# Kernel tuning notes

Measured on AMD Instinct MI355X. Metric: run time of the kernel, lower is better.

The kernel has to match this reference:

```python
import jax, jax.numpy as jnp
import numpy as np
import math

NB_FEATURES = 256

def _softmax_kernel(x, projection_matrix):
    # x: [B,H,N,D], projection_matrix: [D,F] -> [B,H,N,F]
    x_proj = jnp.einsum('bhnd,df->bhnf', x, projection_matrix)
    x_proj = x_proj - jnp.max(x_proj, axis=-1, keepdims=True)
    return jnp.exp(x_proj) / math.sqrt(projection_matrix.shape[-1])

def setup_inputs() -> dict:
    key = jax.random.key(0)
    k1, k2, k3, k4 = jax.random.split(key, 4)
    B, H, N, D = 2, 16, 4096, 64
    q = jax.random.normal(k1, (B, H, N, D), dtype=jnp.float32)
    k = jax.random.normal(k2, (B, H, N, D), dtype=jnp.float32)
    v = jax.random.normal(k3, (B, H, N, D), dtype=jnp.float32)
    projection_matrix = jax.random.normal(k4, (D, NB_FEATURES), dtype=jnp.float32)
    return {"q": q, "k": k, "v": v, "projection_matrix": projection_matrix}

def reference(q, k, v, projection_matrix):
    q_prime = _softmax_kernel(q, projection_matrix)  # [B,H,N,F]
    k_prime = _softmax_kernel(k, projection_matrix)  # [B,H,N,F]
    kv = jnp.einsum('bhnf,bhne->bhfe', k_prime, v)   # [B,H,F,E]
    denom = jnp.einsum('bhnf,bhf->bhn', q_prime, jnp.sum(k_prime, axis=-2) + 1e-06)
    z = 1.0 / denom[..., None]                        # [B,H,N,1]
    out = jnp.einsum('bhnf,bhfe->bhne', q_prime, kv)  # [B,H,N,E]
    return out * z
```

## Files before the change

kernel.cpp:

```cpp
#include <hip/hip_runtime.h>
#include <math.h>

typedef float f4 __attribute__((ext_vector_type(4)));
typedef float f32x4 __attribute__((ext_vector_type(4)));
typedef _Float16 h4 __attribute__((ext_vector_type(4)));
typedef _Float16 h8 __attribute__((ext_vector_type(8)));

#define BH 32
#define NN 4096
#define DD 64
#define FF 256
#define EE 64
#define SPLITS 8
#define ROWS_K 512
#define QB 8
#define ROWS_Q 512
#define ST 72
#define SK 136
#define STF 264

#define MFMA(a, b, c) __builtin_amdgcn_mfma_f32_16x16x32_f16((a), (b), (c), 0, 0, 0)

__device__ inline h8 cvt2(f4 x0, f4 x1) {
  h8 r;
  r[0] = (_Float16)x0.x; r[1] = (_Float16)x0.y;
  r[2] = (_Float16)x0.z; r[3] = (_Float16)x0.w;
  r[4] = (_Float16)x1.x; r[5] = (_Float16)x1.y;
  r[6] = (_Float16)x1.z; r[7] = (_Float16)x1.w;
  return r;
}

__global__ __launch_bounds__(512, 2) void fa_kside(
    const float* __restrict__ kin, const float* __restrict__ vin,
    const float* __restrict__ P, float* __restrict__ kv_part,
    float* __restrict__ ksum_part) {
  __shared__ _Float16 Pt[FF * ST];
  __shared__ _Float16 kpt[FF * SK];
  __shared__ _Float16 vt[EE * SK];
  __shared__ float ks_lds[8 * FF];

  const int t = threadIdx.x;
  const int w = t >> 6, lane = t & 63;
  const int g = lane >> 4, fl = lane & 15;
  const int bh = blockIdx.x >> 3, split = blockIdx.x & 7;
  const int bhs = blockIdx.x;
  const int k0 = g * 8;

  {
    const f4* Pg4 = (const f4*)P;
#pragma unroll
    for (int i = 0; i < 8; ++i) {
      int idx = t + i * 512;
      f4 pv = Pg4[idx];
      int d = idx >> 6, f0 = (idx & 63) * 4;
      Pt[(f0 + 0) * ST + d] = (_Float16)pv.x;
      Pt[(f0 + 1) * ST + d] = (_Float16)pv.y;
      Pt[(f0 + 2) * ST + d] = (_Float16)pv.z;
      Pt[(f0 + 3) * ST + d] = (_Float16)pv.w;
    }
  }

  f32x4 kvacc[2][4];
#pragma unroll
  for (int mi = 0; mi < 2; ++mi)
#pragma unroll
    for (int nt = 0; nt < 4; ++nt) kvacc[mi][nt] = (f32x4){0.f, 0.f, 0.f, 0.f};
  float ksum_acc[16];
#pragma unroll
  for (int T = 0; T < 16; ++T) ksum_acc[T] = 0.f;

  const size_t base = (size_t)bh * NN * DD + (size_t)split * ROWS_K * DD;
  __syncthreads();

  for (int tile = 0; tile < 4; ++tile) {
    if (tile) __syncthreads();
    const int r0g = tile * 128 + w * 16;

    const float* krow = kin + base + (size_t)(r0g + fl) * DD;
    h8 a0 = cvt2(*(const f4*)&krow[k0], *(const f4*)&krow[k0 + 4]);
    h8 a1 = cvt2(*(const f4*)&krow[32 + k0], *(const f4*)&krow[32 + k0 + 4]);

    {
      const float* vb = vin + base + (size_t)r0g * DD + lane;
      h8 tv0, tv1;
#pragma unroll
      for (int j = 0; j < 8; ++j) tv0[j] = (_Float16)vb[j * DD];
#pragma unroll
      for (int j = 0; j < 8; ++j) tv1[j] = (_Float16)vb[(8 + j) * DD];
      *(h8*)&vt[lane * SK + w * 16] = tv0;
      *(h8*)&vt[lane * SK + w * 16 + 8] = tv1;
    }

    f32x4 lac[16];
#pragma unroll
    for (int T = 0; T < 16; ++T) {
      int ncol = T * 16 + fl;
      h8 b0 = *(const h8*)&Pt[ncol * ST + k0];
      h8 b1 = *(const h8*)&Pt[ncol * ST + 32 + k0];
      f32x4 c = {0.f, 0.f, 0.f, 0.f};
      c = MFMA(a0, b0, c);
      c = MFMA(a1, b1, c);
      lac[T] = c;
    }

    float mrow[4];
#pragma unroll
    for (int rg = 0; rg < 4; ++rg) {
      float m = lac[0][rg];
#pragma unroll
      for (int T = 1; T < 16; ++T) m = fmaxf(m, lac[T][rg]);
#pragma unroll
      for (int off = 1; off <= 8; off <<= 1)
        m = fmaxf(m, __shfl_xor(m, off, 64));
      mrow[rg] = m;
    }

#pragma unroll
    for (int T = 0; T < 16; ++T) {
      int ncol = T * 16 + fl;
      h4 kp;
#pragma unroll
      for (int rg = 0; rg < 4; ++rg) {
        float ev = __expf(lac[T][rg] - mrow[rg]) * 0.0625f;
        _Float16 hv = (_Float16)ev;
        ksum_acc[T] += (float)hv;
        kp[rg] = hv;
      }
      *(h4*)&kpt[ncol * SK + w * 16 + g * 4] = kp;
    }
    __syncthreads();

#pragma unroll
    for (int kst = 0; kst < 4; ++kst) {
      h8 vbf[4];
#pragma unroll
      for (int nt = 0; nt < 4; ++nt)
        vbf[nt] = *(const h8*)&vt[(nt * 16 + fl) * SK + kst * 32 + k0];
#pragma unroll
      for (int mi = 0; mi < 2; ++mi) {
        h8 ka = *(const h8*)&kpt[((2 * w + mi) * 16 + fl) * SK + kst * 32 + k0];
#pragma unroll
        for (int nt = 0; nt < 4; ++nt)
          kvacc[mi][nt] = MFMA(ka, vbf[nt], kvacc[mi][nt]);
      }
    }
  }

  float* kvp = kv_part + (size_t)bhs * (FF * EE);
#pragma unroll
  for (int mi = 0; mi < 2; ++mi)
#pragma unroll
    for (int nt = 0; nt < 4; ++nt)
#pragma unroll
      for (int rg = 0; rg < 4; ++rg) {
        int f = (2 * w + mi) * 16 + g * 4 + rg;
        int e = nt * 16 + fl;
        kvp[f * EE + e] = kvacc[mi][nt][rg];
      }

#pragma unroll
  for (int T = 0; T < 16; ++T) {
    float s = ksum_acc[T];
    s += __shfl_xor(s, 16, 64);
    s += __shfl_xor(s, 32, 64);
    if (lane < 16) ks_lds[w * FF + T * 16 + lane] = s;
  }
  __syncthreads();
  if (t < FF) {
    float s = 0.f;
#pragma unroll
    for (int wi = 0; wi < 8; ++wi) s += ks_lds[wi * FF + t];
    ksum_part[(size_t)bhs * FF + t] = s;
  }
}

__global__ __launch_bounds__(256) void fa_reduce(
    const float* __restrict__ kv_part, const float* __restrict__ ksum_part,
    _Float16* __restrict__ kvt_g, float* __restrict__ ksum_g) {
  __shared__ _Float16 tl[EE * 18];
  const int b = blockIdx.x, t = threadIdx.x;
  if (b < 512) {
    const int bh = b >> 4, c = b & 15;
#pragma unroll
    for (int i = 0; i < 4; ++i) {
      int idx = i * 256 + t;
      int fr = idx >> 6, e = idx & 63;
      float s = 0.f;
#pragma unroll
      for (int sp = 0; sp < SPLITS; ++sp)
        s += kv_part[(size_t)(bh * SPLITS + sp) * (FF * EE) + (c * 16 + fr) * EE + e];
      tl[e * 18 + fr] = (_Float16)s;
    }
    __syncthreads();
    unsigned int* og = (unsigned int*)kvt_g + (size_t)bh * 8192;
#pragma unroll
    for (int i = 0; i < 2; ++i) {
      int idx = i * 256 + t;
      int e = idx >> 3, fp = (idx & 7) * 2;
      og[e * 128 + c * 8 + (idx & 7)] = *(unsigned int*)&tl[e * 18 + fp];
    }
  } else {
    const int bh = b - 512;
    float s = 0.f;
#pragma unroll
    for (int sp = 0; sp < SPLITS; ++sp)
      s += ksum_part[(size_t)(bh * SPLITS + sp) * FF + t];
    ksum_g[bh * FF + t] = s + 1e-6f;
  }
}

__global__ __launch_bounds__(512, 2) void fa_qside(
    const float* __restrict__ qin, const float* __restrict__ P,
    const _Float16* __restrict__ kvt_g, const float* __restrict__ ksum_g,
    float* __restrict__ out) {
  __shared__ _Float16 Pt[FF * ST];
  __shared__ _Float16 kvt[EE * STF];
  __shared__ _Float16 qpt[8 * 16 * STF];

  const int t = threadIdx.x;
  const int w = t >> 6, lane = t & 63;
  const int g = lane >> 4, fl = lane & 15;
  const int bh = blockIdx.x >> 3, qb = blockIdx.x & 7;
  const int k0 = g * 8;

  {
    const f4* Pg4 = (const f4*)P;
#pragma unroll
    for (int i = 0; i < 8; ++i) {
      int idx = t + i * 512;
      f4 pv = Pg4[idx];
      int d = idx >> 6, f0 = (idx & 63) * 4;
      Pt[(f0 + 0) * ST + d] = (_Float16)pv.x;
      Pt[(f0 + 1) * ST + d] = (_Float16)pv.y;
      Pt[(f0 + 2) * ST + d] = (_Float16)pv.z;
      Pt[(f0 + 3) * ST + d] = (_Float16)pv.w;
    }
  }
  {
    const h8* src = (const h8*)(kvt_g + (size_t)bh * FF * EE);
#pragma unroll
    for (int i = 0; i < 4; ++i) {
      int idx = t + i * 512;
      int e = idx >> 5, f0 = (idx & 31) * 8;
      *(h8*)&kvt[e * STF + f0] = src[idx];
    }
  }
  float ksr[16];
#pragma unroll
  for (int T = 0; T < 16; ++T) ksr[T] = ksum_g[bh * FF + T * 16 + fl];
  __syncthreads();

  _Float16* myqpt = qpt + w * 16 * STF;
  const size_t base = (size_t)bh * NN * DD + (size_t)qb * ROWS_Q * DD;
  float* ob = out + (size_t)bh * NN * EE + (size_t)qb * ROWS_Q * EE;

  for (int st = 0; st < 4; ++st) {
    const int r0g = st * 128 + w * 16;
    const float* qrow = qin + base + (size_t)(r0g + fl) * DD;
    h8 a0 = cvt2(*(const f4*)&qrow[k0], *(const f4*)&qrow[k0 + 4]);
    h8 a1 = cvt2(*(const f4*)&qrow[32 + k0], *(const f4*)&qrow[32 + k0 + 4]);

    f32x4 lac[16];
#pragma unroll
    for (int T = 0; T < 16; ++T) {
      int ncol = T * 16 + fl;
      h8 b0 = *(const h8*)&Pt[ncol * ST + k0];
      h8 b1 = *(const h8*)&Pt[ncol * ST + 32 + k0];
      f32x4 c = {0.f, 0.f, 0.f, 0.f};
      c = MFMA(a0, b0, c);
      c = MFMA(a1, b1, c);
      lac[T] = c;
    }

    float mrow[4];
#pragma unroll
    for (int rg = 0; rg < 4; ++rg) {
      float m = lac[0][rg];
#pragma unroll
      for (int T = 1; T < 16; ++T) m = fmaxf(m, lac[T][rg]);
#pragma unroll
      for (int off = 1; off <= 8; off <<= 1)
        m = fmaxf(m, __shfl_xor(m, off, 64));
      mrow[rg] = m;
    }

    float den[4] = {0.f, 0.f, 0.f, 0.f};
#pragma unroll
    for (int T = 0; T < 16; ++T) {
      int ncol = T * 16 + fl;
#pragma unroll
      for (int rg = 0; rg < 4; ++rg) {
        float ev = __expf(lac[T][rg] - mrow[rg]) * 0.0625f;
        _Float16 hv = (_Float16)ev;
        den[rg] += (float)hv * ksr[T];
        myqpt[(g * 4 + rg) * STF + ncol] = hv;
      }
    }
#pragma unroll
    for (int rg = 0; rg < 4; ++rg) {
#pragma unroll
      for (int off = 1; off <= 8; off <<= 1)
        den[rg] += __shfl_xor(den[rg], off, 64);
    }

    f32x4 oacc[4];
#pragma unroll
    for (int nt = 0; nt < 4; ++nt) oacc[nt] = (f32x4){0.f, 0.f, 0.f, 0.f};
#pragma unroll
    for (int kst = 0; kst < 8; ++kst) {
      h8 aq = *(const h8*)&myqpt[fl * STF + kst * 32 + k0];
#pragma unroll
      for (int nt = 0; nt < 4; ++nt) {
        h8 bq = *(const h8*)&kvt[(nt * 16 + fl) * STF + kst * 32 + k0];
        oacc[nt] = MFMA(aq, bq, oacc[nt]);
      }
    }

    float* obt = ob + (size_t)r0g * EE;
#pragma unroll
    for (int rg = 0; rg < 4; ++rg) {
      float inv = 1.0f / den[rg];
#pragma unroll
      for (int nt = 0; nt < 4; ++nt) {
        int e = nt * 16 + fl;
        obt[(g * 4 + rg) * EE + e] = oacc[nt][rg] * inv;
      }
    }
  }
}

extern "C" void kernel_launch(void* const* d_in, const int* in_sizes, int n_in,
                              void* d_out, int out_size, void* d_ws,
                              size_t ws_size, hipStream_t stream) {
  (void)in_sizes;
  (void)n_in;
  (void)out_size;
  (void)ws_size;
  const float* q = (const float*)d_in[0];
  const float* k = (const float*)d_in[1];
  const float* v = (const float*)d_in[2];
  const float* P = (const float*)d_in[3];
  float* out = (float*)d_out;

  float* kv_part = (float*)d_ws;
  float* ksum_part = kv_part + 256 * 16384;
  _Float16* kvt_g = (_Float16*)(ksum_part + 256 * 256);
  float* ksum_g = (float*)(kvt_g + 32 * 16384);

  hipLaunchKernelGGL(fa_kside, dim3(BH * SPLITS), dim3(512), 0, stream, k, v, P,
                     kv_part, ksum_part);
  hipLaunchKernelGGL(fa_reduce, dim3(544), dim3(256), 0, stream, kv_part,
                     ksum_part, kvt_g, ksum_g);
  hipLaunchKernelGGL(fa_qside, dim3(BH * QB), dim3(512), 0, stream, q, P, kvt_g,
                     ksum_g, out);
}
```

Before: 174.8 us.

## Double block size by splitting feature dimension across wave pairs

Both the k-side and q-side kernels now launch 1024 threads (16 waves) instead of 512. Each pair of waves shares a 16-row strip and each wave handles half of the 256 features. The row max and the denominator are combined across the pair through small LDS buffers plus extra barriers. The goal is more resident waves per CU, since LDS already limits each CU to one block, so that latency is hidden better. The cost is extra __syncthreads and LDS traffic per tile, and the launch-bounds hint may squeeze registers.

```diff
diff --git a/kernel.cpp b/kernel.cpp
--- a/kernel.cpp
+++ b/kernel.cpp
@@ -30,27 +30,30 @@
   return r;
 }
 
-__global__ __launch_bounds__(512, 2) void fa_kside(
+__global__ __launch_bounds__(1024, 4) void fa_kside(
     const float* __restrict__ kin, const float* __restrict__ vin,
     const float* __restrict__ P, float* __restrict__ kv_part,
     float* __restrict__ ksum_part) {
   __shared__ _Float16 Pt[FF * ST];
   __shared__ _Float16 kpt[FF * SK];
   __shared__ _Float16 vt[EE * SK];
-  __shared__ float ks_lds[8 * FF];
+  __shared__ float mx_lds[8 * 32];
+  __shared__ float ks_lds[16 * 128];
 
   const int t = threadIdx.x;
   const int w = t >> 6, lane = t & 63;
   const int g = lane >> 4, fl = lane & 15;
+  const int s = w >> 1, h = w & 1;
   const int bh = blockIdx.x >> 3, split = blockIdx.x & 7;
   const int bhs = blockIdx.x;
   const int k0 = g * 8;
+  const int fbase = h * 128;
 
   {
     const f4* Pg4 = (const f4*)P;
 #pragma unroll
-    for (int i = 0; i < 8; ++i) {
-      int idx = t + i * 512;
+    for (int i = 0; i < 4; ++i) {
+      int idx = t + i * 1024;
       f4 pv = Pg4[idx];
       int d = idx >> 6, f0 = (idx & 63) * 4;
       Pt[(f0 + 0) * ST + d] = (_Float16)pv.x;
@@ -60,41 +63,36 @@
     }
   }
 
-  f32x4 kvacc[2][4];
-#pragma unroll
-  for (int mi = 0; mi < 2; ++mi)
-#pragma unroll
-    for (int nt = 0; nt < 4; ++nt) kvacc[mi][nt] = (f32x4){0.f, 0.f, 0.f, 0.f};
-  float ksum_acc[16];
-#pragma unroll
-  for (int T = 0; T < 16; ++T) ksum_acc[T] = 0.f;
+  f32x4 kvacc[4];
+#pragma unroll
+  for (int nt = 0; nt < 4; ++nt) kvacc[nt] = (f32x4){0.f, 0.f, 0.f, 0.f};
+  float ksum_acc[8];
+#pragma unroll
+  for (int T = 0; T < 8; ++T) ksum_acc[T] = 0.f;
 
   const size_t base = (size_t)bh * NN * DD + (size_t)split * ROWS_K * DD;
   __syncthreads();
 
   for (int tile = 0; tile < 4; ++tile) {
     if (tile) __syncthreads();
-    const int r0g = tile * 128 + w * 16;
-
-    const float* krow = kin + base + (size_t)(r0g + fl) * DD;
+    const int r0 = tile * 128;
+
+    const float* krow = kin + base + (size_t)(r0 + s * 16 + fl) * DD;
     h8 a0 = cvt2(*(const f4*)&krow[k0], *(const f4*)&krow[k0 + 4]);
     h8 a1 = cvt2(*(const f4*)&krow[32 + k0], *(const f4*)&krow[32 + k0 + 4]);
 
     {
-      const float* vb = vin + base + (size_t)r0g * DD + lane;
-      h8 tv0, tv1;
-#pragma unroll
-      for (int j = 0; j < 8; ++j) tv0[j] = (_Float16)vb[j * DD];
-#pragma unroll
-      for (int j = 0; j < 8; ++j) tv1[j] = (_Float16)vb[(8 + j) * DD];
-      *(h8*)&vt[lane * SK + w * 16] = tv0;
-      *(h8*)&vt[lane * SK + w * 16 + 8] = tv1;
-    }
-
-    f32x4 lac[16];
-#pragma unroll
-    for (int T = 0; T < 16; ++T) {
-      int ncol = T * 16 + fl;
+      const float* vb = vin + base + (size_t)(r0 + w * 8) * DD + lane;
+      h8 tv;
+#pragma unroll
+      for (int j = 0; j < 8; ++j) tv[j] = (_Float16)vb[j * DD];
+      *(h8*)&vt[lane * SK + w * 8] = tv;
+    }
+
+    f32x4 lac[8];
+#pragma unroll
+    for (int T = 0; T < 8; ++T) {
+      int ncol = fbase + T * 16 + fl;
       h8 b0 = *(const h8*)&Pt[ncol * ST + k0];
       h8 b1 = *(const h8*)&Pt[ncol * ST + 32 + k0];
       f32x4 c = {0.f, 0.f, 0.f, 0.f};
@@ -108,16 +106,25 @@
     for (int rg = 0; rg < 4; ++rg) {
       float m = lac[0][rg];
 #pragma unroll
-      for (int T = 1; T < 16; ++T) m = fmaxf(m, lac[T][rg]);
+      for (int T = 1; T < 8; ++T) m = fmaxf(m, lac[T][rg]);
 #pragma unroll
       for (int off = 1; off <= 8; off <<= 1)
         m = fmaxf(m, __shfl_xor(m, off, 64));
       mrow[rg] = m;
     }
-
-#pragma unroll
-    for (int T = 0; T < 16; ++T) {
-      int ncol = T * 16 + fl;
+    if (fl == 0) {
+#pragma unroll
+      for (int rg = 0; rg < 4; ++rg)
+        mx_lds[s * 32 + h * 16 + g * 4 + rg] = mrow[rg];
+    }
+    __syncthreads();
+#pragma unroll
+    for (int rg = 0; rg < 4; ++rg)
+      mrow[rg] = fmaxf(mrow[rg], mx_lds[s * 32 + (1 - h) * 16 + g * 4 + rg]);
+
+#pragma unroll
+    for (int T = 0; T < 8; ++T) {
+      int ncol = fbase + T * 16 + fl;
       h4 kp;
 #pragma unroll
       for (int rg = 0; rg < 4; ++rg) {
@@ -126,7 +133,7 @@
         ksum_acc[T] += (float)hv;
         kp[rg] = hv;
       }
-      *(h4*)&kpt[ncol * SK + w * 16 + g * 4] = kp;
+      *(h4*)&kpt[ncol * SK + s * 16 + g * 4] = kp;
     }
     __syncthreads();
 
@@ -136,41 +143,37 @@
 #pragma unroll
       for (int nt = 0; nt < 4; ++nt)
         vbf[nt] = *(const h8*)&vt[(nt * 16 + fl) * SK + kst * 32 + k0];
-#pragma unroll
-      for (int mi = 0; mi < 2; ++mi) {
-        h8 ka = *(const h8*)&kpt[((2 * w + mi) * 16 + fl) * SK + kst * 32 + k0];
-#pragma unroll
-        for (int nt = 0; nt < 4; ++nt)
-          kvacc[mi][nt] = MFMA(ka, vbf[nt], kvacc[mi][nt]);
-      }
+      h8 ka = *(const h8*)&kpt[(w * 16 + fl) * SK + kst * 32 + k0];
+#pragma unroll
+      for (int nt = 0; nt < 4; ++nt)
+        kvacc[nt] = MFMA(ka, vbf[nt], kvacc[nt]);
     }
   }
 
   float* kvp = kv_part + (size_t)bhs * (FF * EE);
 #pragma unroll
-  for (int mi = 0; mi < 2; ++mi)
-#pragma unroll
-    for (int nt = 0; nt < 4; ++nt)
-#pragma unroll
-      for (int rg = 0; rg < 4; ++rg) {
-        int f = (2 * w + mi) * 16 + g * 4 + rg;
-        int e = nt * 16 + fl;
-        kvp[f * EE + e] = kvacc[mi][nt][rg];
-      }
-
-#pragma unroll
-  for (int T = 0; T < 16; ++T) {
-    float s = ksum_acc[T];
-    s += __shfl_xor(s, 16, 64);
-    s += __shfl_xor(s, 32, 64);
-    if (lane < 16) ks_lds[w * FF + T * 16 + lane] = s;
+  for (int nt = 0; nt < 4; ++nt)
+#pragma unroll
+    for (int rg = 0; rg < 4; ++rg) {
+      int f = w * 16 + g * 4 + rg;
+      int e = nt * 16 + fl;
+      kvp[f * EE + e] = kvacc[nt][rg];
+    }
+
+#pragma unroll
+  for (int T = 0; T < 8; ++T) {
+    float sv = ksum_acc[T];
+    sv += __shfl_xor(sv, 16, 64);
+    sv += __shfl_xor(sv, 32, 64);
+    if (lane < 16) ks_lds[w * 128 + T * 16 + lane] = sv;
   }
   __syncthreads();
   if (t < FF) {
-    float s = 0.f;
-#pragma unroll
-    for (int wi = 0; wi < 8; ++wi) s += ks_lds[wi * FF + t];
-    ksum_part[(size_t)bhs * FF + t] = s;
+    int hh = t >> 7, inner = t & 127;
+    float sv = 0.f;
+#pragma unroll
+    for (int si = 0; si < 8; ++si) sv += ks_lds[(si * 2 + hh) * 128 + inner];
+    ksum_part[(size_t)bhs * FF + t] = sv;
   }
 }
 
@@ -209,25 +212,29 @@
   }
 }
 
-__global__ __launch_bounds__(512, 2) void fa_qside(
+__global__ __launch_bounds__(1024, 4) void fa_qside(
     const float* __restrict__ qin, const float* __restrict__ P,
     const _Float16* __restrict__ kvt_g, const float* __restrict__ ksum_g,
     float* __restrict__ out) {
   __shared__ _Float16 Pt[FF * ST];
   __shared__ _Float16 kvt[EE * STF];
   __shared__ _Float16 qpt[8 * 16 * STF];
+  __shared__ float mx_lds[8 * 32];
+  __shared__ float den_lds[8 * 32];
 
   const int t = threadIdx.x;
   const int w = t >> 6, lane = t & 63;
   const int g = lane >> 4, fl = lane & 15;
+  const int s = w >> 1, h = w & 1;
   const int bh = blockIdx.x >> 3, qb = blockIdx.x & 7;
   const int k0 = g * 8;
+  const int fbase = h * 128;
 
   {
     const f4* Pg4 = (const f4*)P;
 #pragma unroll
-    for (int i = 0; i < 8; ++i) {
-      int idx = t + i * 512;
+    for (int i = 0; i < 4; ++i) {
+      int idx = t + i * 1024;
       f4 pv = Pg4[idx];
       int d = idx >> 6, f0 = (idx & 63) * 4;
       Pt[(f0 + 0) * ST + d] = (_Float16)pv.x;
@@ -239,31 +246,33 @@
   {
     const h8* src = (const h8*)(kvt_g + (size_t)bh * FF * EE);
 #pragma unroll
-    for (int i = 0; i < 4; ++i) {
-      int idx = t + i * 512;
+    for (int i = 0; i < 2; ++i) {
+      int idx = t + i * 1024;
       int e = idx >> 5, f0 = (idx & 31) * 8;
       *(h8*)&kvt[e * STF + f0] = src[idx];
     }
   }
-  float ksr[16];
-#pragma unroll
-  for (int T = 0; T < 16; ++T) ksr[T] = ksum_g[bh * FF + T * 16 + fl];
+  float ksr[8];
+#pragma unroll
+  for (int T = 0; T < 8; ++T)
+    ksr[T] = ksum_g[bh * FF + fbase + T * 16 + fl];
   __syncthreads();
 
-  _Float16* myqpt = qpt + w * 16 * STF;
+  _Float16* myqpt = qpt + s * 16 * STF;
   const size_t base = (size_t)bh * NN * DD + (size_t)qb * ROWS_Q * DD;
   float* ob = out + (size_t)bh * NN * EE + (size_t)qb * ROWS_Q * EE;
 
   for (int st = 0; st < 4; ++st) {
-    const int r0g = st * 128 + w * 16;
-    const float* qrow = qin + base + (size_t)(r0g + fl) * DD;
+    if (st) __syncthreads();
+    const int r0 = st * 128;
+    const float* qrow = qin + base + (size_t)(r0 + s * 16 + fl) * DD;
     h8 a0 = cvt2(*(const f4*)&qrow[k0], *(const f4*)&qrow[k0 + 4]);
     h8 a1 = cvt2(*(const f4*)&qrow[32 + k0], *(const f4*)&qrow[32 + k0 + 4]);
 
-    f32x4 lac[16];
-#pragma unroll
-    for (int T = 0; T < 16; ++T) {
-      int ncol = T * 16 + fl;
+    f32x4 lac[8];
+#pragma unroll
+    for (int T = 0; T < 8; ++T) {
+      int ncol = fbase + T * 16 + fl;
       h8 b0 = *(const h8*)&Pt[ncol * ST + k0];
       h8 b1 = *(const h8*)&Pt[ncol * ST + 32 + k0];
       f32x4 c = {0.f, 0.f, 0.f, 0.f};
@@ -277,17 +286,26 @@
     for (int rg = 0; rg < 4; ++rg) {
       float m = lac[0][rg];
 #pragma unroll
-      for (int T = 1; T < 16; ++T) m = fmaxf(m, lac[T][rg]);
+      for (int T = 1; T < 8; ++T) m = fmaxf(m, lac[T][rg]);
 #pragma unroll
       for (int off = 1; off <= 8; off <<= 1)
         m = fmaxf(m, __shfl_xor(m, off, 64));
       mrow[rg] = m;
     }
+    if (fl == 0) {
+#pragma unroll
+      for (int rg = 0; rg < 4; ++rg)
+        mx_lds[s * 32 + h * 16 + g * 4 + rg] = mrow[rg];
+    }
+    __syncthreads();
+#pragma unroll
+    for (int rg = 0; rg < 4; ++rg)
+      mrow[rg] = fmaxf(mrow[rg], mx_lds[s * 32 + (1 - h) * 16 + g * 4 + rg]);
 
     float den[4] = {0.f, 0.f, 0.f, 0.f};
 #pragma unroll
-    for (int T = 0; T < 16; ++T) {
-      int ncol = T * 16 + fl;
+    for (int T = 0; T < 8; ++T) {
+      int ncol = fbase + T * 16 + fl;
 #pragma unroll
       for (int rg = 0; rg < 4; ++rg) {
         float ev = __expf(lac[T][rg] - mrow[rg]) * 0.0625f;
@@ -302,28 +320,40 @@
       for (int off = 1; off <= 8; off <<= 1)
         den[rg] += __shfl_xor(den[rg], off, 64);
     }
-
-    f32x4 oacc[4];
-#pragma unroll
-    for (int nt = 0; nt < 4; ++nt) oacc[nt] = (f32x4){0.f, 0.f, 0.f, 0.f};
+    if (fl == 0) {
+#pragma unroll
+      for (int rg = 0; rg < 4; ++rg)
+        den_lds[s * 32 + h * 16 + g * 4 + rg] = den[rg];
+    }
+    __syncthreads();
+
+    float inv[4];
+#pragma unroll
+    for (int rg = 0; rg < 4; ++rg) {
+      float dtot = den_lds[s * 32 + g * 4 + rg] + den_lds[s * 32 + 16 + g * 4 + rg];
+      inv[rg] = 1.0f / dtot;
+    }
+
+    f32x4 oacc[2];
+#pragma unroll
+    for (int n2 = 0; n2 < 2; ++n2) oacc[n2] = (f32x4){0.f, 0.f, 0.f, 0.f};
 #pragma unroll
     for (int kst = 0; kst < 8; ++kst) {
       h8 aq = *(const h8*)&myqpt[fl * STF + kst * 32 + k0];
 #pragma unroll
-      for (int nt = 0; nt < 4; ++nt) {
-        h8 bq = *(const h8*)&kvt[(nt * 16 + fl) * STF + kst * 32 + k0];
-        oacc[nt] = MFMA(aq, bq, oacc[nt]);
+      for (int n2 = 0; n2 < 2; ++n2) {
+        h8 bq = *(const h8*)&kvt[((h * 2 + n2) * 16 + fl) * STF + kst * 32 + k0];
+        oacc[n2] = MFMA(aq, bq, oacc[n2]);
       }
     }
 
-    float* obt = ob + (size_t)r0g * EE;
-#pragma unroll
-    for (int rg = 0; rg < 4; ++rg) {
-      float inv = 1.0f / den[rg];
-#pragma unroll
-      for (int nt = 0; nt < 4; ++nt) {
-        int e = nt * 16 + fl;
-        obt[(g * 4 + rg) * EE + e] = oacc[nt][rg] * inv;
+    float* obt = ob + (size_t)(r0 + s * 16) * EE;
+#pragma unroll
+    for (int rg = 0; rg < 4; ++rg) {
+#pragma unroll
+      for (int n2 = 0; n2 < 2; ++n2) {
+        int e = (h * 2 + n2) * 16 + fl;
+        obt[(g * 4 + rg) * EE + e] = oacc[n2][rg] * inv[rg];
       }
     }
   }
@@ -347,10 +377,10 @@
   _Float16* kvt_g = (_Float16*)(ksum_part + 256 * 256);
   float* ksum_g = (float*)(kvt_g + 32 * 16384);
 
-  hipLaunchKernelGGL(fa_kside, dim3(BH * SPLITS), dim3(512), 0, stream, k, v, P,
-                     kv_part, ksum_part);
+  hipLaunchKernelGGL(fa_kside, dim3(BH * SPLITS), dim3(1024), 0, stream, k, v,
+                     P, kv_part, ksum_part);
   hipLaunchKernelGGL(fa_reduce, dim3(544), dim3(256), 0, stream, kv_part,
                      ksum_part, kvt_g, ksum_g);
-  hipLaunchKernelGGL(fa_qside, dim3(BH * QB), dim3(512), 0, stream, q, P, kvt_g,
-                     ksum_g, out);
-}
+  hipLaunchKernelGGL(fa_qside, dim3(BH * QB), dim3(1024), 0, stream, q, P,
+                     kvt_g, ksum_g, out);
+}
```

Measured after the change: 182.1 us. +4.2%, slower.

## Double splits, store fp16 KV partials, keep Q features in registers

Applied to the files above, without the earlier changes.

The K-side kernel now runs 512 blocks of 256 threads over 256-row splits, with an XOR-swizzled LDS layout for the exp(K) tile and KV partials written in fp16. This halves the partial traffic into the reduce step. The Q-side kernel swaps the MFMA operands so each lane holds a full output row's features in registers. The second GEMM uses 16x16x16 MFMA directly from registers, which removes the per-wave LDS staging of q features and lets the kernel target higher occupancy. fp16 partial sums add some rounding error, and the larger split count doubles the reduce's read count.

```diff
diff --git a/kernel.cpp b/kernel.cpp
--- a/kernel.cpp
+++ b/kernel.cpp
@@ -11,15 +11,15 @@
 #define DD 64
 #define FF 256
 #define EE 64
-#define SPLITS 8
-#define ROWS_K 512
-#define QB 8
-#define ROWS_Q 512
+#define SPLITS 16
+#define ROWS_K 256
+#define QB 16
+#define ROWS_Q 256
 #define ST 72
-#define SK 136
 #define STF 264
 
 #define MFMA(a, b, c) __builtin_amdgcn_mfma_f32_16x16x32_f16((a), (b), (c), 0, 0, 0)
+#define MFMA16(a, b, c) __builtin_amdgcn_mfma_f32_16x16x16f16((a), (b), (c), 0, 0, 0)
 
 __device__ inline h8 cvt2(f4 x0, f4 x1) {
   h8 r;
@@ -30,20 +30,204 @@
   return r;
 }
 
-__global__ __launch_bounds__(512, 2) void fa_kside(
+__global__ __launch_bounds__(256, 2) void fa_kside(
     const float* __restrict__ kin, const float* __restrict__ vin,
-    const float* __restrict__ P, float* __restrict__ kv_part,
+    const float* __restrict__ P, _Float16* __restrict__ kv_part,
     float* __restrict__ ksum_part) {
   __shared__ _Float16 Pt[FF * ST];
-  __shared__ _Float16 kpt[FF * SK];
-  __shared__ _Float16 vt[EE * SK];
-  __shared__ float ks_lds[8 * FF];
+  __shared__ _Float16 kpt[FF * 64];
+  __shared__ _Float16 vt[EE * 72];
+  float* ks_lds = (float*)vt;
 
   const int t = threadIdx.x;
   const int w = t >> 6, lane = t & 63;
   const int g = lane >> 4, fl = lane & 15;
-  const int bh = blockIdx.x >> 3, split = blockIdx.x & 7;
+  const int bh = blockIdx.x >> 4, split = blockIdx.x & 15;
   const int bhs = blockIdx.x;
+  const int k0 = g * 8;
+  const int swz = (fl & 7) << 3;
+
+  {
+    const f4* Pg4 = (const f4*)P;
+#pragma unroll
+    for (int i = 0; i < 16; ++i) {
+      int idx = t + i * 256;
+      f4 pv = Pg4[idx];
+      int d = idx >> 6, f0 = (idx & 63) * 4;
+      Pt[(f0 + 0) * ST + d] = (_Float16)pv.x;
+      Pt[(f0 + 1) * ST + d] = (_Float16)pv.y;
+      Pt[(f0 + 2) * ST + d] = (_Float16)pv.z;
+      Pt[(f0 + 3) * ST + d] = (_Float16)pv.w;
+    }
+  }
+
+  f32x4 kvacc[4][4];
+#pragma unroll
+  for (int mi = 0; mi < 4; ++mi)
+#pragma unroll
+    for (int nt = 0; nt < 4; ++nt) kvacc[mi][nt] = (f32x4){0.f, 0.f, 0.f, 0.f};
+  float ksum_acc[16];
+#pragma unroll
+  for (int T = 0; T < 16; ++T) ksum_acc[T] = 0.f;
+
+  const size_t base = (size_t)bh * NN * DD + (size_t)split * ROWS_K * DD;
+  __syncthreads();
+
+  for (int tile = 0; tile < 4; ++tile) {
+    if (tile) __syncthreads();
+    const int r0g = tile * 64 + w * 16;
+
+    const float* krow = kin + base + (size_t)(r0g + fl) * DD;
+    h8 a0 = cvt2(*(const f4*)&krow[k0], *(const f4*)&krow[k0 + 4]);
+    h8 a1 = cvt2(*(const f4*)&krow[32 + k0], *(const f4*)&krow[32 + k0 + 4]);
+
+    {
+      const float* vb = vin + base + (size_t)r0g * DD + lane;
+      h8 tv0, tv1;
+#pragma unroll
+      for (int j = 0; j < 8; ++j) tv0[j] = (_Float16)vb[j * DD];
+#pragma unroll
+      for (int j = 0; j < 8; ++j) tv1[j] = (_Float16)vb[(8 + j) * DD];
+      *(h8*)&vt[lane * 72 + w * 16] = tv0;
+      *(h8*)&vt[lane * 72 + w * 16 + 8] = tv1;
+    }
+
+    f32x4 lac[16];
+#pragma unroll
+    for (int T = 0; T < 16; ++T) {
+      int ncol = T * 16 + fl;
+      h8 b0 = *(const h8*)&Pt[ncol * ST + k0];
+      h8 b1 = *(const h8*)&Pt[ncol * ST + 32 + k0];
+      f32x4 c = {0.f, 0.f, 0.f, 0.f};
+      c = MFMA(a0, b0, c);
+      c = MFMA(a1, b1, c);
+      lac[T] = c;
+    }
+
+    float mrow[4];
+#pragma unroll
+    for (int rg = 0; rg < 4; ++rg) {
+      float m = lac[0][rg];
+#pragma unroll
+      for (int T = 1; T < 16; ++T) m = fmaxf(m, lac[T][rg]);
+#pragma unroll
+      for (int off = 1; off <= 8; off <<= 1)
+        m = fmaxf(m, __shfl_xor(m, off, 64));
+      mrow[rg] = m;
+    }
+
+    const int kcol = (w * 16 + g * 4) ^ swz;
+#pragma unroll
+    for (int T = 0; T < 16; ++T) {
+      int ncol = T * 16 + fl;
+      h4 kp;
+#pragma unroll
+      for (int rg = 0; rg < 4; ++rg) {
+        float ev = __expf(lac[T][rg] - mrow[rg]) * 0.0625f;
+        _Float16 hv = (_Float16)ev;
+        ksum_acc[T] += (float)hv;
+        kp[rg] = hv;
+      }
+      *(h4*)&kpt[ncol * 64 + kcol] = kp;
+    }
+    __syncthreads();
+
+    const int rc0 = (0 * 32 + k0) ^ swz;
+    const int rc1 = (1 * 32 + k0) ^ swz;
+#pragma unroll
+    for (int kst = 0; kst < 2; ++kst) {
+      const int rcs = kst ? rc1 : rc0;
+      h8 vbf[4];
+#pragma unroll
+      for (int nt = 0; nt < 4; ++nt)
+        vbf[nt] = *(const h8*)&vt[(nt * 16 + fl) * 72 + kst * 32 + k0];
+#pragma unroll
+      for (int mi = 0; mi < 4; ++mi) {
+        h8 ka = *(const h8*)&kpt[((4 * w + mi) * 16 + fl) * 64 + rcs];
+#pragma unroll
+        for (int nt = 0; nt < 4; ++nt)
+          kvacc[mi][nt] = MFMA(ka, vbf[nt], kvacc[mi][nt]);
+      }
+    }
+  }
+
+  _Float16* kvp = kv_part + (size_t)bhs * (FF * EE);
+#pragma unroll
+  for (int mi = 0; mi < 4; ++mi)
+#pragma unroll
+    for (int nt = 0; nt < 4; ++nt)
+#pragma unroll
+      for (int rg = 0; rg < 4; ++rg) {
+        int f = (4 * w + mi) * 16 + g * 4 + rg;
+        int e = nt * 16 + fl;
+        kvp[f * EE + e] = (_Float16)kvacc[mi][nt][rg];
+      }
+
+  __syncthreads();
+#pragma unroll
+  for (int T = 0; T < 16; ++T) {
+    float s = ksum_acc[T];
+    s += __shfl_xor(s, 16, 64);
+    s += __shfl_xor(s, 32, 64);
+    if (lane < 16) ks_lds[w * FF + T * 16 + lane] = s;
+  }
+  __syncthreads();
+  {
+    float s = 0.f;
+#pragma unroll
+    for (int wi = 0; wi < 4; ++wi) s += ks_lds[wi * FF + t];
+    ksum_part[(size_t)bhs * FF + t] = s;
+  }
+}
+
+__global__ __launch_bounds__(256) void fa_reduce(
+    const _Float16* __restrict__ kv_part, const float* __restrict__ ksum_part,
+    _Float16* __restrict__ kvt_g, float* __restrict__ ksum_g) {
+  __shared__ _Float16 tl[EE * 18];
+  const int b = blockIdx.x, t = threadIdx.x;
+  if (b < 512) {
+    const int bh = b >> 4, c = b & 15;
+#pragma unroll
+    for (int i = 0; i < 4; ++i) {
+      int idx = i * 256 + t;
+      int fr = idx >> 6, e = idx & 63;
+      float s = 0.f;
+#pragma unroll
+      for (int sp = 0; sp < SPLITS; ++sp)
+        s += (float)kv_part[(size_t)(bh * SPLITS + sp) * (FF * EE) +
+                            (c * 16 + fr) * EE + e];
+      tl[e * 18 + fr] = (_Float16)s;
+    }
+    __syncthreads();
+    unsigned int* og = (unsigned int*)kvt_g + (size_t)bh * 8192;
+#pragma unroll
+    for (int i = 0; i < 2; ++i) {
+      int idx = i * 256 + t;
+      int e = idx >> 3, fp = (idx & 7) * 2;
+      og[e * 128 + c * 8 + (idx & 7)] = *(unsigned int*)&tl[e * 18 + fp];
+    }
+  } else {
+    const int bh = b - 512;
+    float s = 0.f;
+#pragma unroll
+    for (int sp = 0; sp < SPLITS; ++sp)
+      s += ksum_part[(size_t)(bh * SPLITS + sp) * FF + t];
+    ksum_g[bh * FF + t] = s + 1e-6f;
+  }
+}
+
+__global__ __launch_bounds__(512, 4) void fa_qside(
+    const float* __restrict__ qin, const float* __restrict__ P,
+    const _Float16* __restrict__ kvt_g, const float* __restrict__ ksum_g,
+    float* __restrict__ out) {
+  __shared__ _Float16 Pt[FF * ST];
+  __shared__ _Float16 kvt[EE * STF];
+  __shared__ float ks_lds[FF];
+
+  const int t = threadIdx.x;
+  const int w = t >> 6, lane = t & 63;
+  const int g = lane >> 4, fl = lane & 15;
+  const int bh = blockIdx.x >> 4, qb = blockIdx.x & 15;
   const int k0 = g * 8;
 
   {
@@ -59,37 +243,26 @@
       Pt[(f0 + 3) * ST + d] = (_Float16)pv.w;
     }
   }
-
-  f32x4 kvacc[2][4];
-#pragma unroll
-  for (int mi = 0; mi < 2; ++mi)
-#pragma unroll
-    for (int nt = 0; nt < 4; ++nt) kvacc[mi][nt] = (f32x4){0.f, 0.f, 0.f, 0.f};
-  float ksum_acc[16];
-#pragma unroll
-  for (int T = 0; T < 16; ++T) ksum_acc[T] = 0.f;
-
-  const size_t base = (size_t)bh * NN * DD + (size_t)split * ROWS_K * DD;
+  {
+    const h8* src = (const h8*)(kvt_g + (size_t)bh * FF * EE);
+#pragma unroll
+    for (int i = 0; i < 4; ++i) {
+      int idx = t + i * 512;
+      int e = idx >> 5, f0 = (idx & 31) * 8;
+      *(h8*)&kvt[e * STF + f0] = src[idx];
+    }
+  }
+  if (t < FF) ks_lds[t] = ksum_g[bh * FF + t];
   __syncthreads();
 
-  for (int tile = 0; tile < 4; ++tile) {
-    if (tile) __syncthreads();
-    const int r0g = tile * 128 + w * 16;
-
-    const float* krow = kin + base + (size_t)(r0g + fl) * DD;
-    h8 a0 = cvt2(*(const f4*)&krow[k0], *(const f4*)&krow[k0 + 4]);
-    h8 a1 = cvt2(*(const f4*)&krow[32 + k0], *(const f4*)&krow[32 + k0 + 4]);
-
-    {
-      const float* vb = vin + base + (size_t)r0g * DD + lane;
-      h8 tv0, tv1;
-#pragma unroll
-      for (int j = 0; j < 8; ++j) tv0[j] = (_Float16)vb[j * DD];
-#pragma unroll
-      for (int j = 0; j < 8; ++j) tv1[j] = (_Float16)vb[(8 + j) * DD];
-      *(h8*)&vt[lane * SK + w * 16] = tv0;
-      *(h8*)&vt[lane * SK + w * 16 + 8] = tv1;
-    }
+  const size_t base = (size_t)bh * NN * DD + (size_t)qb * ROWS_Q * DD;
+  float* ob = out + (size_t)bh * NN * EE + (size_t)qb * ROWS_Q * EE;
+
+  for (int st = 0; st < 2; ++st) {
+    const int r0g = st * 128 + w * 16;
+    const float* qrow = qin + base + (size_t)(r0g + fl) * DD;
+    h8 a0 = cvt2(*(const f4*)&qrow[k0], *(const f4*)&qrow[k0 + 4]);
+    h8 a1 = cvt2(*(const f4*)&qrow[32 + k0], *(const f4*)&qrow[32 + k0 + 4]);
 
     f32x4 lac[16];
 #pragma unroll
@@ -98,233 +271,55 @@
       h8 b0 = *(const h8*)&Pt[ncol * ST + k0];
       h8 b1 = *(const h8*)&Pt[ncol * ST + 32 + k0];
       f32x4 c = {0.f, 0.f, 0.f, 0.f};
-      c = MFMA(a0, b0, c);
-      c = MFMA(a1, b1, c);
+      c = MFMA(b0, a0, c);
+      c = MFMA(b1, a1, c);
       lac[T] = c;
     }
 
-    float mrow[4];
-#pragma unroll
-    for (int rg = 0; rg < 4; ++rg) {
-      float m = lac[0][rg];
-#pragma unroll
-      for (int T = 1; T < 16; ++T) m = fmaxf(m, lac[T][rg]);
-#pragma unroll
-      for (int off = 1; off <= 8; off <<= 1)
-        m = fmaxf(m, __shfl_xor(m, off, 64));
-      mrow[rg] = m;
-    }
-
+    float m = lac[0][0];
+#pragma unroll
+    for (int T = 0; T < 16; ++T)
+#pragma unroll
+      for (int rg = 0; rg < 4; ++rg) m = fmaxf(m, lac[T][rg]);
+    m = fmaxf(m, __shfl_xor(m, 16, 64));
+    m = fmaxf(m, __shfl_xor(m, 32, 64));
+
+    h4 qp4[16];
+    float den = 0.f;
 #pragma unroll
     for (int T = 0; T < 16; ++T) {
-      int ncol = T * 16 + fl;
-      h4 kp;
+      f4 ksf = *(const f4*)&ks_lds[T * 16 + g * 4];
 #pragma unroll
       for (int rg = 0; rg < 4; ++rg) {
-        float ev = __expf(lac[T][rg] - mrow[rg]) * 0.0625f;
+        float ev = __expf(lac[T][rg] - m) * 0.0625f;
         _Float16 hv = (_Float16)ev;
-        ksum_acc[T] += (float)hv;
-        kp[rg] = hv;
-      }
-      *(h4*)&kpt[ncol * SK + w * 16 + g * 4] = kp;
-    }
-    __syncthreads();
-
-#pragma unroll
-    for (int kst = 0; kst < 4; ++kst) {
-      h8 vbf[4];
-#pragma unroll
-      for (int nt = 0; nt < 4; ++nt)
-        vbf[nt] = *(const h8*)&vt[(nt * 16 + fl) * SK + kst * 32 + k0];
-#pragma unroll
-      for (int mi = 0; mi < 2; ++mi) {
-        h8 ka = *(const h8*)&kpt[((2 * w + mi) * 16 + fl) * SK + kst * 32 + k0];
-#pragma unroll
-        for (int nt = 0; nt < 4; ++nt)
-          kvacc[mi][nt] = MFMA(ka, vbf[nt], kvacc[mi][nt]);
-      }
-    }
-  }
-
-  float* kvp = kv_part + (size_t)bhs * (FF * EE);
-#pragma unroll
-  for (int mi = 0; mi < 2; ++mi)
-#pragma unroll
-    for (int nt = 0; nt < 4; ++nt)
-#pragma unroll
-      for (int rg = 0; rg < 4; ++rg) {
-        int f = (2 * w + mi) * 16 + g * 4 + rg;
-        int e = nt * 16 + fl;
-        kvp[f * EE + e] = kvacc[mi][nt][rg];
-      }
-
-#pragma unroll
-  for (int T = 0; T < 16; ++T) {
-    float s = ksum_acc[T];
-    s += __shfl_xor(s, 16, 64);
-    s += __shfl_xor(s, 32, 64);
-    if (lane < 16) ks_lds[w * FF + T * 16 + lane] = s;
-  }
-  __syncthreads();
-  if (t < FF) {
-    float s = 0.f;
-#pragma unroll
-    for (int wi = 0; wi < 8; ++wi) s += ks_lds[wi * FF + t];
-    ksum_part[(size_t)bhs * FF + t] = s;
-  }
-}
-
-__global__ __launch_bounds__(256) void fa_reduce(
-    const float* __restrict__ kv_part, const float* __restrict__ ksum_part,
-    _Float16* __restrict__ kvt_g, float* __restrict__ ksum_g) {
-  __shared__ _Float16 tl[EE * 18];
-  const int b = blockIdx.x, t = threadIdx.x;
-  if (b < 512) {
-    const int bh = b >> 4, c = b & 15;
-#pragma unroll
-    for (int i = 0; i < 4; ++i) {
-      int idx = i * 256 + t;
-      int fr = idx >> 6, e = idx & 63;
-      float s = 0.f;
-#pragma unroll
-      for (int sp = 0; sp < SPLITS; ++sp)
-        s += kv_part[(size_t)(bh * SPLITS + sp) * (FF * EE) + (c * 16 + fr) * EE + e];
-      tl[e * 18 + fr] = (_Float16)s;
-    }
-    __syncthreads();
-    unsigned int* og = (unsigned int*)kvt_g + (size_t)bh * 8192;
-#pragma unroll
-    for (int i = 0; i < 2; ++i) {
-      int idx = i * 256 + t;
-      int e = idx >> 3, fp = (idx & 7) * 2;
-      og[e * 128 + c * 8 + (idx & 7)] = *(unsigned int*)&tl[e * 18 + fp];
-    }
-  } else {
-    const int bh = b - 512;
-    float s = 0.f;
-#pragma unroll
-    for (int sp = 0; sp < SPLITS; ++sp)
-      s += ksum_part[(size_t)(bh * SPLITS + sp) * FF + t];
-    ksum_g[bh * FF + t] = s + 1e-6f;
-  }
-}
-
-__global__ __launch_bounds__(512, 2) void fa_qside(
-    const float* __restrict__ qin, const float* __restrict__ P,
-    const _Float16* __restrict__ kvt_g, const float* __restrict__ ksum_g,
-    float* __restrict__ out) {
-  __shared__ _Float16 Pt[FF * ST];
-  __shared__ _Float16 kvt[EE * STF];
-  __shared__ _Float16 qpt[8 * 16 * STF];
-
-  const int t = threadIdx.x;
-  const int w = t >> 6, lane = t & 63;
-  const int g = lane >> 4, fl = lane & 15;
-  const int bh = blockIdx.x >> 3, qb = blockIdx.x & 7;
-  const int k0 = g * 8;
-
-  {
-    const f4* Pg4 = (const f4*)P;
-#pragma unroll
-    for (int i = 0; i < 8; ++i) {
-      int idx = t + i * 512;
-      f4 pv = Pg4[idx];
-      int d = idx >> 6, f0 = (idx & 63) * 4;
-      Pt[(f0 + 0) * ST + d] = (_Float16)pv.x;
-      Pt[(f0 + 1) * ST + d] = (_Float16)pv.y;
-      Pt[(f0 + 2) * ST + d] = (_Float16)pv.z;
-      Pt[(f0 + 3) * ST + d] = (_Float16)pv.w;
-    }
-  }
-  {
-    const h8* src = (const h8*)(kvt_g + (size_t)bh * FF * EE);
-#pragma unroll
-    for (int i = 0; i < 4; ++i) {
-      int idx = t + i * 512;
-      int e = idx >> 5, f0 = (idx & 31) * 8;
-      *(h8*)&kvt[e * STF + f0] = src[idx];
-    }
-  }
-  float ksr[16];
-#pragma unroll
-  for (int T = 0; T < 16; ++T) ksr[T] = ksum_g[bh * FF + T * 16 + fl];
-  __syncthreads();
-
-  _Float16* myqpt = qpt + w * 16 * STF;
-  const size_t base = (size_t)bh * NN * DD + (size_t)qb * ROWS_Q * DD;
-  float* ob = out + (size_t)bh * NN * EE + (size_t)qb * ROWS_Q * EE;
-
-  for (int st = 0; st < 4; ++st) {
-    const int r0g = st * 128 + w * 16;
-    const float* qrow = qin + base + (size_t)(r0g + fl) * DD;
-    h8 a0 = cvt2(*(const f4*)&qrow[k0], *(const f4*)&qrow[k0 + 4]);
-    h8 a1 = cvt2(*(const f4*)&qrow[32 + k0], *(const f4*)&qrow[32 + k0 + 4]);
-
-    f32x4 lac[16];
-#pragma unroll
-    for (int T = 0; T < 16; ++T) {
-      int ncol = T * 16 + fl;
-      h8 b0 = *(const h8*)&Pt[ncol * ST + k0];
-      h8 b1 = *(const h8*)&Pt[ncol * ST + 32 + k0];
-      f32x4 c = {0.f, 0.f, 0.f, 0.f};
-      c = MFMA(a0, b0, c);
-      c = MFMA(a1, b1, c);
-      lac[T] = c;
-    }
-
-    float mrow[4];
-#pragma unroll
-    for (int rg = 0; rg < 4; ++rg) {
-      float m = lac[0][rg];
-#pragma unroll
-      for (int T = 1; T < 16; ++T) m = fmaxf(m, lac[T][rg]);
-#pragma unroll
-      for (int off = 1; off <= 8; off <<= 1)
-        m = fmaxf(m, __shfl_xor(m, off, 64));
-      mrow[rg] = m;
-    }
-
-    float den[4] = {0.f, 0.f, 0.f, 0.f};
-#pragma unroll
-    for (int T = 0; T < 16; ++T) {
-      int ncol = T * 16 + fl;
-#pragma unroll
-      for (int rg = 0; rg < 4; ++rg) {
-        float ev = __expf(lac[T][rg] - mrow[rg]) * 0.0625f;
-        _Float16 hv = (_Float16)ev;
-        den[rg] += (float)hv * ksr[T];
-        myqpt[(g * 4 + rg) * STF + ncol] = hv;
-      }
-    }
-#pragma unroll
-    for (int rg = 0; rg < 4; ++rg) {
-#pragma unroll
-      for (int off = 1; off <= 8; off <<= 1)
-        den[rg] += __shfl_xor(den[rg], off, 64);
-    }
+        den += (float)hv * ksf[rg];
+        qp4[T][rg] = hv;
+      }
+    }
+    den += __shfl_xor(den, 16, 64);
+    den += __shfl_xor(den, 32, 64);
+    const float inv = 1.0f / den;
 
     f32x4 oacc[4];
 #pragma unroll
     for (int nt = 0; nt < 4; ++nt) oacc[nt] = (f32x4){0.f, 0.f, 0.f, 0.f};
 #pragma unroll
-    for (int kst = 0; kst < 8; ++kst) {
-      h8 aq = *(const h8*)&myqpt[fl * STF + kst * 32 + k0];
+    for (int kst = 0; kst < 16; ++kst) {
 #pragma unroll
       for (int nt = 0; nt < 4; ++nt) {
-        h8 bq = *(const h8*)&kvt[(nt * 16 + fl) * STF + kst * 32 + k0];
-        oacc[nt] = MFMA(aq, bq, oacc[nt]);
-      }
-    }
-
-    float* obt = ob + (size_t)r0g * EE;
-#pragma unroll
-    for (int rg = 0; rg < 4; ++rg) {
-      float inv = 1.0f / den[rg];
-#pragma unroll
-      for (int nt = 0; nt < 4; ++nt) {
-        int e = nt * 16 + fl;
-        obt[(g * 4 + rg) * EE + e] = oacc[nt][rg] * inv;
-      }
+        h4 av = *(const h4*)&kvt[(nt * 16 + fl) * STF + kst * 16 + g * 4];
+        oacc[nt] = MFMA16(av, qp4[kst], oacc[nt]);
+      }
+    }
+
+    float* obt = ob + (size_t)(r0g + fl) * EE;
+#pragma unroll
+    for (int nt = 0; nt < 4; ++nt) {
+      f4 o;
+#pragma unroll
+      for (int rg = 0; rg < 4; ++rg) o[rg] = oacc[nt][rg] * inv;
+      *(f4*)&obt[nt * 16 + g * 4] = o;
     }
   }
 }
@@ -342,12 +337,12 @@
   const float* P = (const float*)d_in[3];
   float* out = (float*)d_out;
 
-  float* kv_part = (float*)d_ws;
-  float* ksum_part = kv_part + 256 * 16384;
-  _Float16* kvt_g = (_Float16*)(ksum_part + 256 * 256);
+  _Float16* kv_part = (_Float16*)d_ws;
+  float* ksum_part = (float*)(kv_part + 512 * 16384);
+  _Float16* kvt_g = (_Float16*)(ksum_part + 512 * 256);
   float* ksum_g = (float*)(kvt_g + 32 * 16384);
 
-  hipLaunchKernelGGL(fa_kside, dim3(BH * SPLITS), dim3(512), 0, stream, k, v, P,
+  hipLaunchKernelGGL(fa_kside, dim3(BH * SPLITS), dim3(256), 0, stream, k, v, P,
                      kv_part, ksum_part);
   hipLaunchKernelGGL(fa_reduce, dim3(544), dim3(256), 0, stream, kv_part,
                      ksum_part, kvt_g, ksum_g);
```

New measurement: 344.1 us. 1.97x slower.

## Split K-side into 16 chunks of 256-thread blocks with fp16 partials and swizzled LDS

Applied to the files above, without the earlier changes.

Restructures the K-side kernel to use 16 splits of 256 rows with 256-thread blocks, each wave now accumulating 64 feature rows of the kv partial. The kv partials are stored as fp16 instead of fp32 to halve the partial write and reduce traffic, and the k' LDS tile drops its padding in favour of an XOR swizzle to avoid bank conflicts. The ksum scratch reuses the V tile buffer to cut LDS use. It doubles the number of partials the reduce kernel sums and adds fp16 rounding to the partial sums.

```diff
diff --git a/kernel.cpp b/kernel.cpp
--- a/kernel.cpp
+++ b/kernel.cpp
@@ -11,12 +11,11 @@
 #define DD 64
 #define FF 256
 #define EE 64
-#define SPLITS 8
-#define ROWS_K 512
+#define SPLITS 16
+#define ROWS_K 256
 #define QB 8
 #define ROWS_Q 512
 #define ST 72
-#define SK 136
 #define STF 264
 
 #define MFMA(a, b, c) __builtin_amdgcn_mfma_f32_16x16x32_f16((a), (b), (c), 0, 0, 0)
@@ -30,27 +29,28 @@
   return r;
 }
 
-__global__ __launch_bounds__(512, 2) void fa_kside(
+__global__ __launch_bounds__(256, 2) void fa_kside(
     const float* __restrict__ kin, const float* __restrict__ vin,
-    const float* __restrict__ P, float* __restrict__ kv_part,
+    const float* __restrict__ P, _Float16* __restrict__ kv_part,
     float* __restrict__ ksum_part) {
   __shared__ _Float16 Pt[FF * ST];
-  __shared__ _Float16 kpt[FF * SK];
-  __shared__ _Float16 vt[EE * SK];
-  __shared__ float ks_lds[8 * FF];
+  __shared__ _Float16 kpt[FF * 64];
+  __shared__ _Float16 vt[EE * 72];
+  float* ks_lds = (float*)vt;
 
   const int t = threadIdx.x;
   const int w = t >> 6, lane = t & 63;
   const int g = lane >> 4, fl = lane & 15;
-  const int bh = blockIdx.x >> 3, split = blockIdx.x & 7;
+  const int bh = blockIdx.x >> 4, split = blockIdx.x & 15;
   const int bhs = blockIdx.x;
   const int k0 = g * 8;
+  const int swz = (fl & 7) << 3;
 
   {
     const f4* Pg4 = (const f4*)P;
 #pragma unroll
-    for (int i = 0; i < 8; ++i) {
-      int idx = t + i * 512;
+    for (int i = 0; i < 16; ++i) {
+      int idx = t + i * 256;
       f4 pv = Pg4[idx];
       int d = idx >> 6, f0 = (idx & 63) * 4;
       Pt[(f0 + 0) * ST + d] = (_Float16)pv.x;
@@ -60,9 +60,9 @@
     }
   }
 
-  f32x4 kvacc[2][4];
-#pragma unroll
-  for (int mi = 0; mi < 2; ++mi)
+  f32x4 kvacc[4][4];
+#pragma unroll
+  for (int mi = 0; mi < 4; ++mi)
 #pragma unroll
     for (int nt = 0; nt < 4; ++nt) kvacc[mi][nt] = (f32x4){0.f, 0.f, 0.f, 0.f};
   float ksum_acc[16];
@@ -74,7 +74,7 @@
 
   for (int tile = 0; tile < 4; ++tile) {
     if (tile) __syncthreads();
-    const int r0g = tile * 128 + w * 16;
+    const int r0g = tile * 64 + w * 16;
 
     const float* krow = kin + base + (size_t)(r0g + fl) * DD;
     h8 a0 = cvt2(*(const f4*)&krow[k0], *(const f4*)&krow[k0 + 4]);
@@ -87,8 +87,8 @@
       for (int j = 0; j < 8; ++j) tv0[j] = (_Float16)vb[j * DD];
 #pragma unroll
       for (int j = 0; j < 8; ++j) tv1[j] = (_Float16)vb[(8 + j) * DD];
-      *(h8*)&vt[lane * SK + w * 16] = tv0;
-      *(h8*)&vt[lane * SK + w * 16 + 8] = tv1;
+      *(h8*)&vt[lane * 72 + w * 16] = tv0;
+      *(h8*)&vt[lane * 72 + w * 16 + 8] = tv1;
     }
 
     f32x4 lac[16];
@@ -115,6 +115,7 @@
       mrow[rg] = m;
     }
 
+    const int kcol = (w * 16 + g * 4) ^ swz;
 #pragma unroll
     for (int T = 0; T < 16; ++T) {
       int ncol = T * 16 + fl;
@@ -126,19 +127,22 @@
         ksum_acc[T] += (float)hv;
         kp[rg] = hv;
       }
-      *(h4*)&kpt[ncol * SK + w * 16 + g * 4] = kp;
+      *(h4*)&kpt[ncol * 64 + kcol] = kp;
     }
     __syncthreads();
 
-#pragma unroll
-    for (int kst = 0; kst < 4; ++kst) {
+    const int rc0 = (0 * 32 + k0) ^ swz;
+    const int rc1 = (1 * 32 + k0) ^ swz;
+#pragma unroll
+    for (int kst = 0; kst < 2; ++kst) {
+      const int rcs = kst ? rc1 : rc0;
       h8 vbf[4];
 #pragma unroll
       for (int nt = 0; nt < 4; ++nt)
-        vbf[nt] = *(const h8*)&vt[(nt * 16 + fl) * SK + kst * 32 + k0];
-#pragma unroll
-      for (int mi = 0; mi < 2; ++mi) {
-        h8 ka = *(const h8*)&kpt[((2 * w + mi) * 16 + fl) * SK + kst * 32 + k0];
+        vbf[nt] = *(const h8*)&vt[(nt * 16 + fl) * 72 + kst * 32 + k0];
+#pragma unroll
+      for (int mi = 0; mi < 4; ++mi) {
+        h8 ka = *(const h8*)&kpt[((4 * w + mi) * 16 + fl) * 64 + rcs];
 #pragma unroll
         for (int nt = 0; nt < 4; ++nt)
           kvacc[mi][nt] = MFMA(ka, vbf[nt], kvacc[mi][nt]);
@@ -146,18 +150,19 @@
     }
   }
 
-  float* kvp = kv_part + (size_t)bhs * (FF * EE);
-#pragma unroll
-  for (int mi = 0; mi < 2; ++mi)
+  _Float16* kvp = kv_part + (size_t)bhs * (FF * EE);
+#pragma unroll
+  for (int mi = 0; mi < 4; ++mi)
 #pragma unroll
     for (int nt = 0; nt < 4; ++nt)
 #pragma unroll
       for (int rg = 0; rg < 4; ++rg) {
-        int f = (2 * w + mi) * 16 + g * 4 + rg;
+        int f = (4 * w + mi) * 16 + g * 4 + rg;
         int e = nt * 16 + fl;
-        kvp[f * EE + e] = kvacc[mi][nt][rg];
-      }
-
+        kvp[f * EE + e] = (_Float16)kvacc[mi][nt][rg];
+      }
+
+  __syncthreads();
 #pragma unroll
   for (int T = 0; T < 16; ++T) {
     float s = ksum_acc[T];
@@ -166,16 +171,16 @@
     if (lane < 16) ks_lds[w * FF + T * 16 + lane] = s;
   }
   __syncthreads();
-  if (t < FF) {
+  {
     float s = 0.f;
 #pragma unroll
-    for (int wi = 0; wi < 8; ++wi) s += ks_lds[wi * FF + t];
+    for (int wi = 0; wi < 4; ++wi) s += ks_lds[wi * FF + t];
     ksum_part[(size_t)bhs * FF + t] = s;
   }
 }
 
 __global__ __launch_bounds__(256) void fa_reduce(
-    const float* __restrict__ kv_part, const float* __restrict__ ksum_part,
+    const _Float16* __restrict__ kv_part, const float* __restrict__ ksum_part,
     _Float16* __restrict__ kvt_g, float* __restrict__ ksum_g) {
   __shared__ _Float16 tl[EE * 18];
   const int b = blockIdx.x, t = threadIdx.x;
@@ -188,7 +193,8 @@
       float s = 0.f;
 #pragma unroll
       for (int sp = 0; sp < SPLITS; ++sp)
-        s += kv_part[(size_t)(bh * SPLITS + sp) * (FF * EE) + (c * 16 + fr) * EE + e];
+        s += (float)kv_part[(size_t)(bh * SPLITS + sp) * (FF * EE) +
+                            (c * 16 + fr) * EE + e];
       tl[e * 18 + fr] = (_Float16)s;
     }
     __syncthreads();
@@ -342,12 +348,12 @@
   const float* P = (const float*)d_in[3];
   float* out = (float*)d_out;
 
-  float* kv_part = (float*)d_ws;
-  float* ksum_part = kv_part + 256 * 16384;
-  _Float16* kvt_g = (_Float16*)(ksum_part + 256 * 256);
+  _Float16* kv_part = (_Float16*)d_ws;
+  float* ksum_part = (float*)(kv_part + 512 * 16384);
+  _Float16* kvt_g = (_Float16*)(ksum_part + 512 * 256);
   float* ksum_g = (float*)(kvt_g + 32 * 16384);
 
-  hipLaunchKernelGGL(fa_kside, dim3(BH * SPLITS), dim3(512), 0, stream, k, v, P,
+  hipLaunchKernelGGL(fa_kside, dim3(BH * SPLITS), dim3(256), 0, stream, k, v, P,
                      kv_part, ksum_part);
   hipLaunchKernelGGL(fa_reduce, dim3(544), dim3(256), 0, stream, kv_part,
                      ksum_part, kvt_g, ksum_g);
```

New measurement: 177.3 us. No clear change (+1.4%).
